# Kernel tuning notes

Hardware: AMD Instinct MI355X
Metric: run time of the kernel (lower is better)

Reference implementation:

```python
import jax, jax.numpy as jnp
import numpy as np

C = 1.0                      # ball curvature c
SQRT_C = 1.0                 # sqrt(c)
EPS = 1e-15                  # norm clamp
BALL_EPS = 1e-5              # projection margin
B, DIN, DOUT = 262144, 128, 128


def artanh(u):
    u = jnp.clip(u, -1.0 + 1e-7, 1.0 - 1e-7)
    return 0.5 * (jnp.log1p(u) - jnp.log1p(-u))


def mobius_matvec(W, x):
    # x: [B, din], W: [dout, din]
    x_norm = jnp.clip(jnp.linalg.norm(x, axis=-1, keepdims=True), EPS)
    Mx = x @ W.T                                   # [B, dout]
    Mx_norm = jnp.clip(jnp.linalg.norm(Mx, axis=-1, keepdims=True), EPS)
    scale = jnp.tanh(Mx_norm / x_norm * artanh(SQRT_C * x_norm)) / (Mx_norm * SQRT_C)
    res = scale * Mx
    return jnp.where(Mx_norm <= 1e-10, 0.0, res)


def mobius_add(x, y):
    # x: [B, d], y broadcastable to [B, d]
    x2 = jnp.sum(x * x, axis=-1, keepdims=True)
    y2 = jnp.sum(y * y, axis=-1, keepdims=True)
    xy = jnp.sum(x * y, axis=-1, keepdims=True)
    num = (1.0 + 2.0 * C * xy + C * y2) * x + (1.0 - C * x2) * y
    den = jnp.clip(1.0 + 2.0 * C * xy + C * C * x2 * y2, EPS)
    return num / den


def projx(x):
    norm = jnp.clip(jnp.linalg.norm(x, axis=-1, keepdims=True), EPS)
    maxnorm = (1.0 - BALL_EPS) / SQRT_C
    return jnp.where(norm > maxnorm, x / norm * maxnorm, x)


def setup_inputs() -> dict:
    key = jax.random.key(0)
    k1, k2, k3 = jax.random.split(key, 3)
    # points strictly inside the unit ball: randn * 0.05 -> norm ~ 0.57 max tail-safe
    x = jax.random.normal(k1, (B, DIN), dtype=jnp.float32) * 0.05
    fan = np.sqrt(6.0 / (DIN + DOUT))  # xavier_uniform scale
    weight = jax.random.uniform(k2, (DOUT, DIN), dtype=jnp.float32, minval=-fan, maxval=fan)
    bias = jax.random.normal(k3, (DOUT,), dtype=jnp.float32) * 0.05
    return {"x": x, "weight": weight, "bias": bias}


def reference(x, weight, bias):
    y = mobius_matvec(weight, x)
    y = mobius_add(y, bias[None, :])
    return projx(y)
```

## Files before the change

kernel.cpp:

```cpp
#include <hip/hip_runtime.h>

typedef __attribute__((ext_vector_type(8))) short short8;
typedef __attribute__((ext_vector_type(4))) float floatx4;

__device__ __forceinline__ unsigned short f2b(float f) {
    union { float f; unsigned int i; } v; v.f = f;
    unsigned int u = v.i;
    u += 0x7FFFu + ((u >> 16) & 1u);
    return (unsigned short)(u >> 16);
}

#define NTILES 2048
#define GRID   1024

__global__ __launch_bounds__(256, 3) void mobius_linear_kernel(
    const float* __restrict__ X,
    const float* __restrict__ W,
    const float* __restrict__ Bias,
    float* __restrict__ Out)
{
    __shared__ unsigned short ldsW[128 * 136];
    __shared__ float ldsB[128];

    const int tid  = threadIdx.x;
    const int wave = tid >> 6;
    const int lane = tid & 63;
    const int q = lane >> 4;
    const int c = lane & 15;

    auto loadx = [&](int T, short8 (&xf)[2][4], float (&xn)[2]) {
        const int rb = T * 128 + wave * 32;
        xn[0] = 0.f; xn[1] = 0.f;
#pragma unroll
        for (int g = 0; g < 2; ++g) {
            const float* xrow = X + (size_t)(rb + g * 16 + c) * 128;
#pragma unroll
            for (int kc = 0; kc < 4; ++kc) {
                const floatx4* src = reinterpret_cast<const floatx4*>(xrow + kc * 32 + q * 8);
                floatx4 x0 = __builtin_nontemporal_load(src);
                floatx4 x1 = __builtin_nontemporal_load(src + 1);
                short8 pk;
#pragma unroll
                for (int j = 0; j < 4; ++j) {
                    xn[g] = fmaf(x0[j], x0[j], xn[g]);
                    xn[g] = fmaf(x1[j], x1[j], xn[g]);
                    pk[j] = (short)f2b(x0[j]); pk[4 + j] = (short)f2b(x1[j]);
                }
                xf[g][kc] = pk;
            }
        }
        xn[0] += __shfl_xor(xn[0], 16); xn[0] += __shfl_xor(xn[0], 32);
        xn[1] += __shfl_xor(xn[1], 16); xn[1] += __shfl_xor(xn[1], 32);
    };

    auto stage_w = [&]() {
#pragma unroll
        for (int i = 0; i < 8; ++i) {
            int chunk = i * 256 + tid;
            int row = chunk >> 4, cc = chunk & 15;
            const float* src = W + row * 128 + cc * 8;
            floatx4 w0 = *reinterpret_cast<const floatx4*>(src);
            floatx4 w1 = *reinterpret_cast<const floatx4*>(src + 4);
            short8 pk;
#pragma unroll
            for (int j = 0; j < 4; ++j) { pk[j] = (short)f2b(w0[j]); pk[4 + j] = (short)f2b(w1[j]); }
            *reinterpret_cast<short8*>(&ldsW[row * 136 + cc * 8]) = pk;
        }
    };

    short8 xfA[2][4], xfB[2][4];
    float xnA[2], xnB[2];
    const int t0 = blockIdx.x;
    const int t1 = blockIdx.x + GRID;

    if (blockIdx.x & 1) { loadx(t0, xfA, xnA); stage_w(); }
    else                { stage_w(); loadx(t0, xfA, xnA); }

    if (tid < 32)
        *reinterpret_cast<floatx4*>(&ldsB[tid * 4]) =
            *reinterpret_cast<const floatx4*>(Bias + tid * 4);

    __syncthreads();

    float b2 = 0.f;
#pragma unroll
    for (int n = 0; n < 8; ++n) {
        floatx4 bv = *reinterpret_cast<const floatx4*>(&ldsB[n * 16 + q * 4]);
#pragma unroll
        for (int r = 0; r < 4; ++r) b2 = fmaf(bv[r], bv[r], b2);
    }
    b2 += __shfl_xor(b2, 16); b2 += __shfl_xor(b2, 32);

    floatx4 acc[2][8];

    auto mfma_all = [&](short8 (&xf)[2][4]) {
#pragma unroll
        for (int g = 0; g < 2; ++g)
#pragma unroll
            for (int n = 0; n < 8; ++n)
                acc[g][n] = (floatx4){0.f, 0.f, 0.f, 0.f};
#pragma unroll
        for (int kc = 0; kc < 4; ++kc) {
#pragma unroll
            for (int n = 0; n < 8; ++n) {
                short8 wf = *reinterpret_cast<const short8*>(
                    &ldsW[(n * 16 + c) * 136 + kc * 32 + q * 8]);
                acc[0][n] = __builtin_amdgcn_mfma_f32_16x16x32_bf16(wf, xf[0][kc], acc[0][n], 0, 0, 0);
                acc[1][n] = __builtin_amdgcn_mfma_f32_16x16x32_bf16(wf, xf[1][kc], acc[1][n], 0, 0, 0);
            }
        }
    };

    auto epilogue = [&](int T, float (&xn)[2]) {
        const int rb = T * 128 + wave * 32;
        floatx4 bfr[8];
#pragma unroll
        for (int n = 0; n < 8; ++n)
            bfr[n] = *reinterpret_cast<const floatx4*>(&ldsB[n * 16 + q * 4]);
#pragma unroll
        for (int g = 0; g < 2; ++g) {
            float m2 = 0.f, mbv = 0.f;
#pragma unroll
            for (int n = 0; n < 8; ++n)
#pragma unroll
                for (int r = 0; r < 4; ++r) {
                    float v = acc[g][n][r];
                    m2  = fmaf(v, v, m2);
                    mbv = fmaf(v, bfr[n][r], mbv);
                }
            m2  += __shfl_xor(m2, 16);  m2  += __shfl_xor(m2, 32);
            mbv += __shfl_xor(mbv, 16); mbv += __shfl_xor(mbv, 32);

            float xnorm = fmaxf(sqrtf(xn[g]), 1e-15f);
            float u     = fminf(xnorm, 1.f - 1e-7f);
            float at    = 0.5f * __logf((1.f + u) / (1.f - u));
            float Mxn   = fmaxf(sqrtf(m2), 1e-15f);
            float arg   = Mxn / xnorm * at;
            float e     = __expf(2.f * arg);
            float th    = 1.f - 2.f / (e + 1.f);
            float scale = (Mxn <= 1e-10f) ? 0.f : th / Mxn;
            float y2 = scale * scale * m2;
            float yb = scale * mbv;
            float t1v = 1.f + 2.f * yb + b2;
            float den = fmaxf(fmaf(y2, b2, 1.f + 2.f * yb), 1e-15f);
            float Af = t1v * scale / den;
            float Bf = (1.f - y2) / den;
            float zn2 = Af * Af * m2 + 2.f * Af * Bf * mbv + Bf * Bf * b2;
            float zn  = fmaxf(sqrtf(zn2), 1e-15f);
            const float maxn = 1.f - 1e-5f;
            float fac = (zn > maxn) ? (maxn / zn) : 1.f;
            Af *= fac; Bf *= fac;

            float* orow = Out + (size_t)(rb + g * 16 + c) * 128;
#pragma unroll
            for (int n = 0; n < 8; ++n) {
                floatx4 o;
#pragma unroll
                for (int r = 0; r < 4; ++r)
                    o[r] = fmaf(Af, acc[g][n][r], Bf * bfr[n][r]);
                *reinterpret_cast<floatx4*>(orow + n * 16 + q * 4) = o;
            }
        }
    };

    mfma_all(xfA);
    loadx(t1, xfB, xnB);
    epilogue(t0, xnA);
    mfma_all(xfB);
    epilogue(t1, xnB);
}

extern "C" void kernel_launch(void* const* d_in, const int* in_sizes, int n_in,
                              void* d_out, int out_size, void* d_ws, size_t ws_size,
                              hipStream_t stream) {
    const float* X    = (const float*)d_in[0];
    const float* W    = (const float*)d_in[1];
    const float* Bias = (const float*)d_in[2];
    float* Out = (float*)d_out;

    dim3 grid(GRID), block(256);
    hipLaunchKernelGGL(mobius_linear_kernel, grid, block, 0, stream, X, W, Bias, Out);
}
```

Before: 259.3 us.

## Use one tile per block with XOR-swizzled W in LDS and higher occupancy

Each block now handles a single 128-row tile and the grid doubles to 2048, which drops the two-tile software pipeline where the second tile's X load overlapped the first tile's epilogue. The LDS padding for W is replaced by an XOR swizzle, bias is read straight from global memory instead of being staged in LDS, and launch bounds rise to 5 blocks per SM. The aim is to hide memory latency through more resident waves rather than in-block prefetch, at the cost of converting and staging W twice as many times across the grid.

```diff
diff --git a/kernel.cpp b/kernel.cpp
--- a/kernel.cpp
+++ b/kernel.cpp
@@ -11,16 +11,15 @@
 }
 
 #define NTILES 2048
-#define GRID   1024
+#define GRID   2048
 
-__global__ __launch_bounds__(256, 3) void mobius_linear_kernel(
+__global__ __launch_bounds__(256, 5) void mobius_linear_kernel(
     const float* __restrict__ X,
     const float* __restrict__ W,
     const float* __restrict__ Bias,
     float* __restrict__ Out)
 {
-    __shared__ unsigned short ldsW[128 * 136];
-    __shared__ float ldsB[128];
+    __shared__ unsigned short ldsW[128 * 128];
 
     const int tid  = threadIdx.x;
     const int wave = tid >> 6;
@@ -28,7 +27,9 @@
     const int q = lane >> 4;
     const int c = lane & 15;
 
-    auto loadx = [&](int T, short8 (&xf)[2][4], float (&xn)[2]) {
+    short8 xf[2][4];
+    float xn[2];
+    auto loadx = [&](int T) {
         const int rb = T * 128 + wave * 32;
         xn[0] = 0.f; xn[1] = 0.f;
 #pragma unroll
@@ -64,110 +65,93 @@
             short8 pk;
 #pragma unroll
             for (int j = 0; j < 4; ++j) { pk[j] = (short)f2b(w0[j]); pk[4 + j] = (short)f2b(w1[j]); }
-            *reinterpret_cast<short8*>(&ldsW[row * 136 + cc * 8]) = pk;
+            *reinterpret_cast<short8*>(&ldsW[row * 128 + ((cc ^ (row & 15)) * 8)]) = pk;
         }
     };
 
-    short8 xfA[2][4], xfB[2][4];
-    float xnA[2], xnB[2];
     const int t0 = blockIdx.x;
-    const int t1 = blockIdx.x + GRID;
 
-    if (blockIdx.x & 1) { loadx(t0, xfA, xnA); stage_w(); }
-    else                { stage_w(); loadx(t0, xfA, xnA); }
-
-    if (tid < 32)
-        *reinterpret_cast<floatx4*>(&ldsB[tid * 4]) =
-            *reinterpret_cast<const floatx4*>(Bias + tid * 4);
+    if (blockIdx.x & 1) { loadx(t0); stage_w(); }
+    else                { stage_w(); loadx(t0); }
 
     __syncthreads();
 
     float b2 = 0.f;
 #pragma unroll
     for (int n = 0; n < 8; ++n) {
-        floatx4 bv = *reinterpret_cast<const floatx4*>(&ldsB[n * 16 + q * 4]);
+        floatx4 bv = *reinterpret_cast<const floatx4*>(Bias + n * 16 + q * 4);
 #pragma unroll
         for (int r = 0; r < 4; ++r) b2 = fmaf(bv[r], bv[r], b2);
     }
     b2 += __shfl_xor(b2, 16); b2 += __shfl_xor(b2, 32);
 
     floatx4 acc[2][8];
-
-    auto mfma_all = [&](short8 (&xf)[2][4]) {
 #pragma unroll
-        for (int g = 0; g < 2; ++g)
-#pragma unroll
-            for (int n = 0; n < 8; ++n)
-                acc[g][n] = (floatx4){0.f, 0.f, 0.f, 0.f};
-#pragma unroll
-        for (int kc = 0; kc < 4; ++kc) {
-#pragma unroll
-            for (int n = 0; n < 8; ++n) {
-                short8 wf = *reinterpret_cast<const short8*>(
-                    &ldsW[(n * 16 + c) * 136 + kc * 32 + q * 8]);
-                acc[0][n] = __builtin_amdgcn_mfma_f32_16x16x32_bf16(wf, xf[0][kc], acc[0][n], 0, 0, 0);
-                acc[1][n] = __builtin_amdgcn_mfma_f32_16x16x32_bf16(wf, xf[1][kc], acc[1][n], 0, 0, 0);
-            }
-        }
-    };
-
-    auto epilogue = [&](int T, float (&xn)[2]) {
-        const int rb = T * 128 + wave * 32;
-        floatx4 bfr[8];
+    for (int g = 0; g < 2; ++g)
 #pragma unroll
         for (int n = 0; n < 8; ++n)
-            bfr[n] = *reinterpret_cast<const floatx4*>(&ldsB[n * 16 + q * 4]);
+            acc[g][n] = (floatx4){0.f, 0.f, 0.f, 0.f};
 #pragma unroll
-        for (int g = 0; g < 2; ++g) {
-            float m2 = 0.f, mbv = 0.f;
+    for (int kc = 0; kc < 4; ++kc) {
 #pragma unroll
-            for (int n = 0; n < 8; ++n)
+        for (int n = 0; n < 8; ++n) {
+            short8 wf = *reinterpret_cast<const short8*>(
+                &ldsW[(n * 16 + c) * 128 + (((kc * 4 + q) ^ c) * 8)]);
+            acc[0][n] = __builtin_amdgcn_mfma_f32_16x16x32_bf16(wf, xf[0][kc], acc[0][n], 0, 0, 0);
+            acc[1][n] = __builtin_amdgcn_mfma_f32_16x16x32_bf16(wf, xf[1][kc], acc[1][n], 0, 0, 0);
+        }
+    }
+
+    const int rb = t0 * 128 + wave * 32;
+    floatx4 bfr[8];
 #pragma unroll
-                for (int r = 0; r < 4; ++r) {
-                    float v = acc[g][n][r];
-                    m2  = fmaf(v, v, m2);
-                    mbv = fmaf(v, bfr[n][r], mbv);
-                }
-            m2  += __shfl_xor(m2, 16);  m2  += __shfl_xor(m2, 32);
-            mbv += __shfl_xor(mbv, 16); mbv += __shfl_xor(mbv, 32);
+    for (int n = 0; n < 8; ++n)
+        bfr[n] = *reinterpret_cast<const floatx4*>(Bias + n * 16 + q * 4);
 
-            float xnorm = fmaxf(sqrtf(xn[g]), 1e-15f);
-            float u     = fminf(xnorm, 1.f - 1e-7f);
-            float at    = 0.5f * __logf((1.f + u) / (1.f - u));
-            float Mxn   = fmaxf(sqrtf(m2), 1e-15f);
-            float arg   = Mxn / xnorm * at;
-            float e     = __expf(2.f * arg);
-            float th    = 1.f - 2.f / (e + 1.f);
-            float scale = (Mxn <= 1e-10f) ? 0.f : th / Mxn;
-            float y2 = scale * scale * m2;
-            float yb = scale * mbv;
-            float t1v = 1.f + 2.f * yb + b2;
-            float den = fmaxf(fmaf(y2, b2, 1.f + 2.f * yb), 1e-15f);
-            float Af = t1v * scale / den;
-            float Bf = (1.f - y2) / den;
-            float zn2 = Af * Af * m2 + 2.f * Af * Bf * mbv + Bf * Bf * b2;
-            float zn  = fmaxf(sqrtf(zn2), 1e-15f);
-            const float maxn = 1.f - 1e-5f;
-            float fac = (zn > maxn) ? (maxn / zn) : 1.f;
-            Af *= fac; Bf *= fac;
+#pragma unroll
+    for (int g = 0; g < 2; ++g) {
+        float m2 = 0.f, mbv = 0.f;
+#pragma unroll
+        for (int n = 0; n < 8; ++n)
+#pragma unroll
+            for (int r = 0; r < 4; ++r) {
+                float v = acc[g][n][r];
+                m2  = fmaf(v, v, m2);
+                mbv = fmaf(v, bfr[n][r], mbv);
+            }
+        m2  += __shfl_xor(m2, 16);  m2  += __shfl_xor(m2, 32);
+        mbv += __shfl_xor(mbv, 16); mbv += __shfl_xor(mbv, 32);
 
-            float* orow = Out + (size_t)(rb + g * 16 + c) * 128;
+        float xnorm = fmaxf(sqrtf(xn[g]), 1e-15f);
+        float u     = fminf(xnorm, 1.f - 1e-7f);
+        float at    = 0.5f * __logf((1.f + u) / (1.f - u));
+        float Mxn   = fmaxf(sqrtf(m2), 1e-15f);
+        float arg   = Mxn / xnorm * at;
+        float e     = __expf(2.f * arg);
+        float th    = 1.f - 2.f / (e + 1.f);
+        float scale = (Mxn <= 1e-10f) ? 0.f : th / Mxn;
+        float y2 = scale * scale * m2;
+        float yb = scale * mbv;
+        float t1v = 1.f + 2.f * yb + b2;
+        float den = fmaxf(fmaf(y2, b2, 1.f + 2.f * yb), 1e-15f);
+        float Af = t1v * scale / den;
+        float Bf = (1.f - y2) / den;
+        float zn2 = Af * Af * m2 + 2.f * Af * Bf * mbv + Bf * Bf * b2;
+        float zn  = fmaxf(sqrtf(zn2), 1e-15f);
+        const float maxn = 1.f - 1e-5f;
+        float fac = (zn > maxn) ? (maxn / zn) : 1.f;
+        Af *= fac; Bf *= fac;
+
+        float* orow = Out + (size_t)(rb + g * 16 + c) * 128;
 #pragma unroll
-            for (int n = 0; n < 8; ++n) {
-                floatx4 o;
+        for (int n = 0; n < 8; ++n) {
+            floatx4 o;
 #pragma unroll
-                for (int r = 0; r < 4; ++r)
-                    o[r] = fmaf(Af, acc[g][n][r], Bf * bfr[n][r]);
-                *reinterpret_cast<floatx4*>(orow + n * 16 + q * 4) = o;
-            }
+            for (int r = 0; r < 4; ++r)
+                o[r] = fmaf(Af, acc[g][n][r], Bf * bfr[n][r]);
+            *reinterpret_cast<floatx4*>(orow + n * 16 + q * 4) = o;
         }
-    };
-
-    mfma_all(xfA);
-    loadx(t1, xfB, xnB);
-    epilogue(t0, xnA);
-    mfma_all(xfB);
-    epilogue(t1, xnB);
+    }
 }
 
 extern "C" void kernel_launch(void* const* d_in, const int* in_sizes, int n_in,
```

Measured after the change: 294.4 us. 13.6% more time.
